# Performance work log

Hardware: AMD Instinct MI355X
Metric: run time of the kernel (lower is better)

The kernel has to match this reference:

```python
import jax, jax.numpy as jnp
import numpy as np

B, H, S, D = 4, 16, 8192, 64

def setup_inputs() -> dict:
    key0 = jax.random.key(0)
    kq, kk, kv = jax.random.split(key0, 3)
    query = jax.random.normal(kq, (B, H, S, D), dtype=jnp.float32)
    key = jax.random.normal(kk, (B, H, S, D), dtype=jnp.float32)
    value = jax.random.normal(kv, (B, H, S, D), dtype=jnp.float32)
    return {"query": query, "key": key, "value": value}

def reference(query, key, value):
    phi_q = jax.nn.relu(query)            # [B,H,S,D]
    phi_k = jax.nn.relu(key)              # [B,H,S,D]
    kv = jnp.einsum('bhsd,bhse->bhde', phi_k, value)   # [B,H,D,D]
    out = jnp.einsum('bhsd,bhde->bhse', phi_q, kv)      # [B,H,S,D]
    k_sum = phi_k.sum(axis=-2)            # [B,H,D]
    normalizer = jnp.einsum('bhsd,bhd->bhs', phi_q, k_sum)[..., None]  # [B,H,S,1]
    normalizer = jnp.maximum(normalizer, 1e-6)
    return out / normalizer
```

## Files before the change

### kernel.cpp

```cpp
#include <hip/hip_runtime.h>


#define NBH 64
#define SEQ 8192
#define DIM 64
#define NSPLIT 16
#define ROWS_A (SEQ / NSPLIT)
#define TILE_A 32
#define KV_STRIDE (DIM * DIM + DIM)

__global__ __launch_bounds__(256) void la_kv(const float* __restrict__ K,
                                             const float* __restrict__ V,
                                             float* __restrict__ ws) {
    const int t = threadIdx.x;
    const int bh = blockIdx.x >> 4;
    const int chunk = blockIdx.x & (NSPLIT - 1);
    const int td = t >> 4;
    const int te = t & 15;

    __shared__ float sk[TILE_A * DIM];
    __shared__ float sv[TILE_A * DIM];

    float acc[4][4] = {};
    float ks[4] = {0.f, 0.f, 0.f, 0.f};

    const int base = bh * (SEQ * DIM) + chunk * (ROWS_A * DIM);
    const float4* K4 = reinterpret_cast<const float4*>(K + base);
    const float4* V4 = reinterpret_cast<const float4*>(V + base);

    for (int tile = 0; tile < ROWS_A / TILE_A; ++tile) {
        const int f0 = tile * (TILE_A * DIM / 4);
        float4 ka = K4[f0 + t];
        float4 kb = K4[f0 + t + 256];
        float4 va = V4[f0 + t];
        float4 vb = V4[f0 + t + 256];
        ka.x = fmaxf(ka.x, 0.f); ka.y = fmaxf(ka.y, 0.f);
        ka.z = fmaxf(ka.z, 0.f); ka.w = fmaxf(ka.w, 0.f);
        kb.x = fmaxf(kb.x, 0.f); kb.y = fmaxf(kb.y, 0.f);
        kb.z = fmaxf(kb.z, 0.f); kb.w = fmaxf(kb.w, 0.f);
        ks[0] += ka.x + kb.x; ks[1] += ka.y + kb.y;
        ks[2] += ka.z + kb.z; ks[3] += ka.w + kb.w;
        __syncthreads();
        *reinterpret_cast<float4*>(&sk[t * 4]) = ka;
        *reinterpret_cast<float4*>(&sk[1024 + t * 4]) = kb;
        *reinterpret_cast<float4*>(&sv[t * 4]) = va;
        *reinterpret_cast<float4*>(&sv[1024 + t * 4]) = vb;
        __syncthreads();
        #pragma unroll 8
        for (int ss = 0; ss < TILE_A; ++ss) {
            float4 kk = *reinterpret_cast<const float4*>(&sk[ss * DIM + td * 4]);
            float4 vv = *reinterpret_cast<const float4*>(&sv[ss * DIM + te * 4]);
            acc[0][0] = fmaf(kk.x, vv.x, acc[0][0]);
            acc[0][1] = fmaf(kk.x, vv.y, acc[0][1]);
            acc[0][2] = fmaf(kk.x, vv.z, acc[0][2]);
            acc[0][3] = fmaf(kk.x, vv.w, acc[0][3]);
            acc[1][0] = fmaf(kk.y, vv.x, acc[1][0]);
            acc[1][1] = fmaf(kk.y, vv.y, acc[1][1]);
            acc[1][2] = fmaf(kk.y, vv.z, acc[1][2]);
            acc[1][3] = fmaf(kk.y, vv.w, acc[1][3]);
            acc[2][0] = fmaf(kk.z, vv.x, acc[2][0]);
            acc[2][1] = fmaf(kk.z, vv.y, acc[2][1]);
            acc[2][2] = fmaf(kk.z, vv.z, acc[2][2]);
            acc[2][3] = fmaf(kk.z, vv.w, acc[2][3]);
            acc[3][0] = fmaf(kk.w, vv.x, acc[3][0]);
            acc[3][1] = fmaf(kk.w, vv.y, acc[3][1]);
            acc[3][2] = fmaf(kk.w, vv.z, acc[3][2]);
            acc[3][3] = fmaf(kk.w, vv.w, acc[3][3]);
        }
    }

    float* w = ws + bh * KV_STRIDE;
    #pragma unroll
    for (int i = 0; i < 4; ++i)
        #pragma unroll
        for (int j = 0; j < 4; ++j)
            atomicAdd(&w[(td * 4 + i) * DIM + te * 4 + j], acc[i][j]);

    #pragma unroll
    for (int c = 0; c < 4; ++c) {
        ks[c] += __shfl_xor(ks[c], 16);
        ks[c] += __shfl_xor(ks[c], 32);
    }
    if ((t & 48) == 0) {
        #pragma unroll
        for (int c = 0; c < 4; ++c)
            atomicAdd(&w[DIM * DIM + te * 4 + c], ks[c]);
    }
}

#define TILES_B 8
#define TILE_B 64
#define QPAD 68

__global__ __launch_bounds__(256) void la_out(const float* __restrict__ Q,
                                              const float* __restrict__ ws,
                                              float* __restrict__ out) {
    const int t = threadIdx.x;
    const int bh = blockIdx.x >> 4;
    const int chunk = blockIdx.x & 15;
    const int sr = t >> 2;
    const int te = t & 3;

    __shared__ float skv[DIM * DIM];
    __shared__ float sks[DIM];
    __shared__ float sq[TILE_B * QPAD];
    __shared__ float sinv[TILE_B];

    const float* w = ws + bh * KV_STRIDE;
    #pragma unroll
    for (int i = 0; i < 4; ++i)
        *reinterpret_cast<float4*>(&skv[(t + i * 256) * 4]) =
            *reinterpret_cast<const float4*>(&w[(t + i * 256) * 4]);
    if (t < 16)
        *reinterpret_cast<float4*>(&sks[t * 4]) =
            *reinterpret_cast<const float4*>(&w[DIM * DIM + t * 4]);

    const int rowbase0 = chunk * (TILES_B * TILE_B);
    const float* Qb = Q + bh * (SEQ * DIM);
    float* Ob = out + bh * (SEQ * DIM);

    for (int tile = 0; tile < TILES_B; ++tile) {
        const int rb = rowbase0 + tile * TILE_B;
        __syncthreads();
        #pragma unroll
        for (int i = 0; i < 4; ++i) {
            const int idx = t + i * 256;
            float4 q4 = *reinterpret_cast<const float4*>(&Qb[rb * DIM + idx * 4]);
            q4.x = fmaxf(q4.x, 0.f); q4.y = fmaxf(q4.y, 0.f);
            q4.z = fmaxf(q4.z, 0.f); q4.w = fmaxf(q4.w, 0.f);
            const int row = idx >> 4;
            const int d0 = (idx & 15) * 4;
            *reinterpret_cast<float4*>(&sq[row * QPAD + d0]) = q4;
        }
        __syncthreads();
        if (t < TILE_B) {
            float n = 0.f;
            #pragma unroll
            for (int d4 = 0; d4 < 16; ++d4) {
                float4 q4 = *reinterpret_cast<const float4*>(&sq[t * QPAD + d4 * 4]);
                float4 k4 = *reinterpret_cast<const float4*>(&sks[d4 * 4]);
                n = fmaf(q4.x, k4.x, n); n = fmaf(q4.y, k4.y, n);
                n = fmaf(q4.z, k4.z, n); n = fmaf(q4.w, k4.w, n);
            }
            sinv[t] = 1.0f / fmaxf(n, 1e-6f);
        }
        __syncthreads();

        float o[4][4] = {};
        #pragma unroll 16
        for (int d = 0; d < DIM; ++d) {
            const float qd = sq[sr * QPAD + d];
            #pragma unroll
            for (int i = 0; i < 4; ++i) {
                float4 kv4 = *reinterpret_cast<const float4*>(
                    &skv[d * DIM + i * 16 + te * 4]);
                o[i][0] = fmaf(qd, kv4.x, o[i][0]);
                o[i][1] = fmaf(qd, kv4.y, o[i][1]);
                o[i][2] = fmaf(qd, kv4.z, o[i][2]);
                o[i][3] = fmaf(qd, kv4.w, o[i][3]);
            }
        }
        const float inv = sinv[sr];
        #pragma unroll
        for (int i = 0; i < 4; ++i) {
            float4 r;
            r.x = o[i][0] * inv; r.y = o[i][1] * inv;
            r.z = o[i][2] * inv; r.w = o[i][3] * inv;
            *reinterpret_cast<float4*>(&Ob[(rb + sr) * DIM + i * 16 + te * 4]) = r;
        }
    }
}

extern "C" void kernel_launch(void* const* d_in, const int* in_sizes, int n_in,
                              void* d_out, int out_size, void* d_ws, size_t ws_size,
                              hipStream_t stream) {
    const float* Q = (const float*)d_in[0];
    const float* K = (const float*)d_in[1];
    const float* V = (const float*)d_in[2];
    float* out = (float*)d_out;
    float* ws = (float*)d_ws;

    hipMemsetAsync(ws, 0, (size_t)NBH * KV_STRIDE * sizeof(float), stream);

    la_kv<<<NBH * NSPLIT, 256, 0, stream>>>(K, V, ws);
    la_out<<<NBH * NSPLIT, 256, 0, stream>>>(Q, ws, out);
}
```

Before: 494.4 us.

## Prefetch K/V tiles into registers, drop Q staging in shared memory, double grid splits

The KV-accumulation kernel now loads the next K/V tile into registers while the current tile is being reduced from shared memory. The output kernel reads each Q row directly from global memory per thread and computes the normalizer inline. This removes the shared Q tile and the per-tile barriers. Both kernels use twice as many blocks, with occupancy hints added to launch bounds, which doubles the atomic traffic into the workspace. The risk is that the four threads sharing a row each read the full 256-byte Q row uncoalesced, leaning on cache for reuse.

```diff
diff --git a/kernel.cpp b/kernel.cpp
--- a/kernel.cpp
+++ b/kernel.cpp
@@ -4,17 +4,19 @@
 #define NBH 64
 #define SEQ 8192
 #define DIM 64
-#define NSPLIT 16
-#define ROWS_A (SEQ / NSPLIT)
-#define TILE_A 32
 #define KV_STRIDE (DIM * DIM + DIM)
 
-__global__ __launch_bounds__(256) void la_kv(const float* __restrict__ K,
-                                             const float* __restrict__ V,
-                                             float* __restrict__ ws) {
+#define NSPLIT1 32
+#define ROWS_A (SEQ / NSPLIT1)
+#define TILE_A 32
+#define NTILES_A (ROWS_A / TILE_A)
+
+__global__ __launch_bounds__(256, 8) void la_kv(const float* __restrict__ K,
+                                                const float* __restrict__ V,
+                                                float* __restrict__ ws) {
     const int t = threadIdx.x;
-    const int bh = blockIdx.x >> 4;
-    const int chunk = blockIdx.x & (NSPLIT - 1);
+    const int bh = blockIdx.x >> 5;
+    const int chunk = blockIdx.x & (NSPLIT1 - 1);
     const int td = t >> 4;
     const int te = t & 15;
 
@@ -28,12 +30,10 @@
     const float4* K4 = reinterpret_cast<const float4*>(K + base);
     const float4* V4 = reinterpret_cast<const float4*>(V + base);
 
-    for (int tile = 0; tile < ROWS_A / TILE_A; ++tile) {
-        const int f0 = tile * (TILE_A * DIM / 4);
-        float4 ka = K4[f0 + t];
-        float4 kb = K4[f0 + t + 256];
-        float4 va = V4[f0 + t];
-        float4 vb = V4[f0 + t + 256];
+    float4 ka = K4[t], kb = K4[t + 256];
+    float4 va = V4[t], vb = V4[t + 256];
+
+    for (int tile = 0; tile < NTILES_A; ++tile) {
         ka.x = fmaxf(ka.x, 0.f); ka.y = fmaxf(ka.y, 0.f);
         ka.z = fmaxf(ka.z, 0.f); ka.w = fmaxf(ka.w, 0.f);
         kb.x = fmaxf(kb.x, 0.f); kb.y = fmaxf(kb.y, 0.f);
@@ -46,6 +46,11 @@
         *reinterpret_cast<float4*>(&sv[t * 4]) = va;
         *reinterpret_cast<float4*>(&sv[1024 + t * 4]) = vb;
         __syncthreads();
+        if (tile < NTILES_A - 1) {
+            const int f0 = (tile + 1) * (TILE_A * DIM / 4);
+            ka = K4[f0 + t]; kb = K4[f0 + t + 256];
+            va = V4[f0 + t]; vb = V4[f0 + t + 256];
+        }
         #pragma unroll 8
         for (int ss = 0; ss < TILE_A; ++ss) {
             float4 kk = *reinterpret_cast<const float4*>(&sk[ss * DIM + td * 4]);
@@ -88,23 +93,33 @@
     }
 }
 
-#define TILES_B 8
-#define TILE_B 64
-#define QPAD 68
+#define NSPLIT2 32
+#define ROWS_B (SEQ / NSPLIT2)
 
-__global__ __launch_bounds__(256) void la_out(const float* __restrict__ Q,
-                                              const float* __restrict__ ws,
-                                              float* __restrict__ out) {
+#define DSTEP(qc, dd)                                                          \
+    {                                                                          \
+        const float qv = (qc);                                                 \
+        _Pragma("unroll")                                                      \
+        for (int i = 0; i < 4; ++i) {                                          \
+            float4 kv4 = *reinterpret_cast<const float4*>(                     \
+                &skv[(dd) * DIM + i * 16 + te * 4]);                           \
+            o[i][0] = fmaf(qv, kv4.x, o[i][0]);                                \
+            o[i][1] = fmaf(qv, kv4.y, o[i][1]);                                \
+            o[i][2] = fmaf(qv, kv4.z, o[i][2]);                                \
+            o[i][3] = fmaf(qv, kv4.w, o[i][3]);                                \
+        }                                                                      \
+    }
+
+__global__ __launch_bounds__(256, 8) void la_out(const float* __restrict__ Q,
+                                                 const float* __restrict__ ws,
+                                                 float* __restrict__ out) {
     const int t = threadIdx.x;
-    const int bh = blockIdx.x >> 4;
-    const int chunk = blockIdx.x & 15;
-    const int sr = t >> 2;
+    const int bh = blockIdx.x >> 5;
+    const int chunk = blockIdx.x & (NSPLIT2 - 1);
     const int te = t & 3;
 
     __shared__ float skv[DIM * DIM];
     __shared__ float sks[DIM];
-    __shared__ float sq[TILE_B * QPAD];
-    __shared__ float sinv[TILE_B];
 
     const float* w = ws + bh * KV_STRIDE;
     #pragma unroll
@@ -114,59 +129,37 @@
     if (t < 16)
         *reinterpret_cast<float4*>(&sks[t * 4]) =
             *reinterpret_cast<const float4*>(&w[DIM * DIM + t * 4]);
+    __syncthreads();
 
-    const int rowbase0 = chunk * (TILES_B * TILE_B);
     const float* Qb = Q + bh * (SEQ * DIM);
     float* Ob = out + bh * (SEQ * DIM);
+    const int row0 = chunk * ROWS_B + (t >> 2);
 
-    for (int tile = 0; tile < TILES_B; ++tile) {
-        const int rb = rowbase0 + tile * TILE_B;
-        __syncthreads();
-        #pragma unroll
-        for (int i = 0; i < 4; ++i) {
-            const int idx = t + i * 256;
-            float4 q4 = *reinterpret_cast<const float4*>(&Qb[rb * DIM + idx * 4]);
-            q4.x = fmaxf(q4.x, 0.f); q4.y = fmaxf(q4.y, 0.f);
-            q4.z = fmaxf(q4.z, 0.f); q4.w = fmaxf(q4.w, 0.f);
-            const int row = idx >> 4;
-            const int d0 = (idx & 15) * 4;
-            *reinterpret_cast<float4*>(&sq[row * QPAD + d0]) = q4;
+    for (int iter = 0; iter < ROWS_B / 64; ++iter) {
+        const int row = row0 + iter * 64;
+        const float4* q4p = reinterpret_cast<const float4*>(Qb + row * DIM);
+        float o[4][4] = {};
+        float n = 0.f;
+        #pragma unroll 4
+        for (int d4 = 0; d4 < 16; ++d4) {
+            float4 q = q4p[d4];
+            q.x = fmaxf(q.x, 0.f); q.y = fmaxf(q.y, 0.f);
+            q.z = fmaxf(q.z, 0.f); q.w = fmaxf(q.w, 0.f);
+            float4 k4 = *reinterpret_cast<const float4*>(&sks[d4 * 4]);
+            n = fmaf(q.x, k4.x, n); n = fmaf(q.y, k4.y, n);
+            n = fmaf(q.z, k4.z, n); n = fmaf(q.w, k4.w, n);
+            DSTEP(q.x, d4 * 4 + 0);
+            DSTEP(q.y, d4 * 4 + 1);
+            DSTEP(q.z, d4 * 4 + 2);
+            DSTEP(q.w, d4 * 4 + 3);
         }
-        __syncthreads();
-        if (t < TILE_B) {
-            float n = 0.f;
-            #pragma unroll
-            for (int d4 = 0; d4 < 16; ++d4) {
-                float4 q4 = *reinterpret_cast<const float4*>(&sq[t * QPAD + d4 * 4]);
-                float4 k4 = *reinterpret_cast<const float4*>(&sks[d4 * 4]);
-                n = fmaf(q4.x, k4.x, n); n = fmaf(q4.y, k4.y, n);
-                n = fmaf(q4.z, k4.z, n); n = fmaf(q4.w, k4.w, n);
-            }
-            sinv[t] = 1.0f / fmaxf(n, 1e-6f);
-        }
-        __syncthreads();
-
-        float o[4][4] = {};
-        #pragma unroll 16
-        for (int d = 0; d < DIM; ++d) {
-            const float qd = sq[sr * QPAD + d];
-            #pragma unroll
-            for (int i = 0; i < 4; ++i) {
-                float4 kv4 = *reinterpret_cast<const float4*>(
-                    &skv[d * DIM + i * 16 + te * 4]);
-                o[i][0] = fmaf(qd, kv4.x, o[i][0]);
-                o[i][1] = fmaf(qd, kv4.y, o[i][1]);
-                o[i][2] = fmaf(qd, kv4.z, o[i][2]);
-                o[i][3] = fmaf(qd, kv4.w, o[i][3]);
-            }
-        }
-        const float inv = sinv[sr];
+        const float inv = 1.0f / fmaxf(n, 1e-6f);
         #pragma unroll
         for (int i = 0; i < 4; ++i) {
             float4 r;
             r.x = o[i][0] * inv; r.y = o[i][1] * inv;
             r.z = o[i][2] * inv; r.w = o[i][3] * inv;
-            *reinterpret_cast<float4*>(&Ob[(rb + sr) * DIM + i * 16 + te * 4]) = r;
+            *reinterpret_cast<float4*>(&Ob[row * DIM + i * 16 + te * 4]) = r;
         }
     }
 }
@@ -182,6 +175,6 @@
 
     hipMemsetAsync(ws, 0, (size_t)NBH * KV_STRIDE * sizeof(float), stream);
 
-    la_kv<<<NBH * NSPLIT, 256, 0, stream>>>(K, V, ws);
-    la_out<<<NBH * NSPLIT, 256, 0, stream>>>(Q, ws, out);
+    la_kv<<<NBH * NSPLIT1, 256, 0, stream>>>(K, V, ws);
+    la_out<<<NBH * NSPLIT2, 256, 0, stream>>>(Q, ws, out);
 }
```

After: 549.4 us. +11.1%, slower.
